# Optimization experiments

Hardware: AMD Instinct MI355X
Metric: run time of the kernel (lower is better)

Reference implementation:

```python
import jax, jax.numpy as jnp
import numpy as np


def setup_inputs() -> dict:
    key = jax.random.key(0)
    kK, kV, kQ = jax.random.split(key, 3)
    B, D, S = 4, 64, 4096
    K = jax.random.normal(kK, (B, D, S), dtype=jnp.float32)
    V = jax.random.normal(kV, (B, D, S), dtype=jnp.float32)
    Q = jax.random.normal(kQ, (B, D, S), dtype=jnp.float32)
    return {"K": K, "V": V, "Q": Q}


def reference(K, V, Q):
    # K,V: [B, D, Sk], Q: [B, D, Sq]
    d = Q.shape[1]
    # A[b,k,q] = sum_d K[b,d,k] * Q[b,d,q] / sqrt(d)
    A = jnp.einsum("bdk,bdq->bkq", K, Q) / jnp.sqrt(jnp.asarray(d, Q.dtype))
    A = jax.nn.softmax(A, axis=1)  # normalize over keys (dim 1), matching F.softmax(A, 1)
    # R[b,d,q] = sum_k V[b,d,k] * A[b,k,q]
    R = jnp.einsum("bdk,bkq->bdq", V, A)
    return jnp.concatenate((R, Q), axis=1)  # [B, 2D, Sq]
```

## Files before the change

kernel.cpp:

```cpp
#include <hip/hip_runtime.h>
#include <hip/hip_bf16.h>

#define S_LEN 4096
#define D_DIM 64
#define QB 64
#define KB 32
#define NT (S_LEN / KB)
#define TILE_E 4096
#define WT (NT / 8)

typedef __attribute__((ext_vector_type(8)))  short bf16x8;
typedef __attribute__((ext_vector_type(16))) float f32x16;
typedef unsigned int u32;

#define Z16 {0.f,0.f,0.f,0.f,0.f,0.f,0.f,0.f,0.f,0.f,0.f,0.f,0.f,0.f,0.f,0.f}

union bpack8 { __hip_bfloat16 h[8]; bf16x8 v; };
union ppack  { u32 w[4]; bf16x8 v; };

static __device__ __forceinline__ float fexp2(float x) {
    return __builtin_amdgcn_exp2f(x);
}
static __device__ __forceinline__ u32 cvtpk(float lo, float hi) {
    u32 r;
    asm("v_cvt_pk_bf16_f32 %0, %1, %2" : "=v"(r) : "v"(lo), "v"(hi));
    return r;
}
static __device__ __forceinline__ void plswap(u32 &a, u32 &b) {
    asm("v_permlane32_swap_b32 %0, %1" : "+v"(a), "+v"(b));
}

struct pfrag { ppack p0, p1; };
static __device__ __forceinline__ pfrag packP(const f32x16& s) {
    u32 A = cvtpk(s[0],  s[1]),  Bw = cvtpk(s[2],  s[3]);
    u32 C = cvtpk(s[4],  s[5]),  Dw = cvtpk(s[6],  s[7]);
    u32 E = cvtpk(s[8],  s[9]),  F  = cvtpk(s[10], s[11]);
    u32 G = cvtpk(s[12], s[13]), H  = cvtpk(s[14], s[15]);
    plswap(A, C); plswap(Bw, Dw); plswap(E, G); plswap(F, H);
    pfrag r;
    r.p0.w[0] = A; r.p0.w[1] = Bw; r.p0.w[2] = C; r.p0.w[3] = Dw;
    r.p1.w[0] = E; r.p1.w[1] = F;  r.p1.w[2] = G; r.p1.w[3] = H;
    return r;
}
static __device__ __forceinline__ float treesum(const f32x16& s) {
    float a0 = (s[0] + s[1])   + (s[2] + s[3]);
    float a1 = (s[4] + s[5])   + (s[6] + s[7]);
    float a2 = (s[8] + s[9])   + (s[10] + s[11]);
    float a3 = (s[12] + s[13]) + (s[14] + s[15]);
    return (a0 + a1) + (a2 + a3);
}

#define GLD16(gp, lp) __builtin_amdgcn_global_load_lds( \
    (const __attribute__((address_space(1))) u32*)(const void*)(gp), \
    (__attribute__((address_space(3))) u32*)(void*)(lp), 16, 0, 0)

#define QSCALE 0.18033688011112042f

__global__ __launch_bounds__(256)
void prep_kv(const float* __restrict__ K, const float* __restrict__ V,
             __hip_bfloat16* __restrict__ KVbf)
{
    const int b = blockIdx.y, x = blockIdx.x, z = blockIdx.z;
    const int t = threadIdx.x;

    if (z == 0) {
        const int key = t & 31, dg = t >> 5;
        const float* src = K + ((size_t)b * D_DIM + dg * 8) * S_LEN + x * KB + key;
        bpack8 u;
        #pragma unroll
        for (int e = 0; e < 8; ++e)
            u.h[e] = __float2bfloat16(src[(size_t)e * S_LEN]);
        *(bf16x8*)&KVbf[((size_t)b * NT + x) * TILE_E + t * 8] = u.v;
    } else {
        const int d = t >> 2, kg = t & 3;
        const float* p = V + ((size_t)b * D_DIM + d) * S_LEN + x * KB + kg * 8;
        float4 a = *(const float4*)p, c = *(const float4*)(p + 4);
        bpack8 u;
        u.h[0] = __float2bfloat16(a.x); u.h[1] = __float2bfloat16(a.y);
        u.h[2] = __float2bfloat16(a.z); u.h[3] = __float2bfloat16(a.w);
        u.h[4] = __float2bfloat16(c.x); u.h[5] = __float2bfloat16(c.y);
        u.h[6] = __float2bfloat16(c.z); u.h[7] = __float2bfloat16(c.w);
        *(bf16x8*)&KVbf[((size_t)b * NT + x) * TILE_E + 2048 + (kg * 64 + d) * 8] = u.v;
    }
}

__global__ __launch_bounds__(512, 2)
void attn_fwd(const __hip_bfloat16* __restrict__ KVbf,
              const float* __restrict__ Qg,
              float* __restrict__ out, int swz)
{
    int b, q0;
    if (swz) {
        const int blk = blockIdx.x;
        const int xcd = blk & 7;
        b  = xcd >> 1;
        q0 = (((xcd & 1) << 5) + (blk >> 3)) * QB;
    } else {
        b  = blockIdx.y;
        q0 = blockIdx.x * QB;
    }
    const int t  = threadIdx.x;
    const int lane = t & 63;
    const int w    = t >> 6;
    const int l5   = lane & 31;
    const int h    = lane >> 5;

    __shared__ __align__(16) char Ls[131072];
    char* myL = Ls + w * 16384;

    const __hip_bfloat16* kvb = KVbf + ((size_t)b * NT + w * WT) * TILE_E;
    const float* Qblk = Qg + (size_t)b * D_DIM * S_LEN + q0;

    {
        float* QF = (float*)Ls;
        #pragma unroll
        for (int i = 0; i < 8; ++i) {
            int d = i * 8 + w;
            QF[d * 65 + lane] = Qblk[(size_t)d * S_LEN + lane] * QSCALE;
        }
        __syncthreads();
    }
    bf16x8 qfA[4], qfB[4];
    {
        const float* QF = (const float*)Ls;
        #pragma unroll
        for (int j = 0; j < 4; ++j) {
            float a[8], bq[8];
            #pragma unroll
            for (int e = 0; e < 8; ++e) {
                int dabs = (2 * j + h) * 8 + e;
                a[e]  = QF[dabs * 65 + l5];
                bq[e] = QF[dabs * 65 + 32 + l5];
            }
            ppack pa, pb;
            #pragma unroll
            for (int k2 = 0; k2 < 4; ++k2) {
                pa.w[k2] = cvtpk(a[2 * k2],  a[2 * k2 + 1]);
                pb.w[k2] = cvtpk(bq[2 * k2], bq[2 * k2 + 1]);
            }
            qfA[j] = pa.v;
            qfB[j] = pb.v;
        }
        __syncthreads();
    }

    #pragma unroll
    for (int i = 0; i < 8; ++i)
        GLD16(kvb + i * 512 + lane * 8,          myL + i * 1024);
    #pragma unroll
    for (int i = 0; i < 8; ++i)
        GLD16(kvb + TILE_E + i * 512 + lane * 8, myL + 8192 + i * 1024);

    float lsumA = 0.f, lsumB = 0.f;
    f32x16 accA[2] = {Z16, Z16}, accB[2] = {Z16, Z16};

    for (int it = 0; it < WT; ++it) {
        if (it + 1 < WT) asm volatile("s_waitcnt vmcnt(8)" ::: "memory");
        else             asm volatile("s_waitcnt vmcnt(0)" ::: "memory");
        __builtin_amdgcn_sched_barrier(0);

        const char* Lk = myL + (it & 1) * 8192;
        const char* Lv = Lk + 4096;

        bf16x8 kf[4], vf[4];
        #pragma unroll
        for (int j = 0; j < 4; ++j)
            kf[j] = *(const bf16x8*)(Lk + ((2 * j + h) * 32 + l5) * 16);
        #pragma unroll
        for (int j = 0; j < 2; ++j)
            #pragma unroll
            for (int dt = 0; dt < 2; ++dt)
                vf[2 * j + dt] = *(const bf16x8*)(Lv + ((2 * j + h) * 64 + dt * 32 + l5) * 16);

        f32x16 sA = Z16, sB = Z16;
        __builtin_amdgcn_s_setprio(1);
        #pragma unroll
        for (int j = 0; j < 4; ++j) {
            sA = __builtin_amdgcn_mfma_f32_32x32x16_bf16(kf[j], qfA[j], sA, 0, 0, 0);
            sB = __builtin_amdgcn_mfma_f32_32x32x16_bf16(kf[j], qfB[j], sB, 0, 0, 0);
        }
        __builtin_amdgcn_s_setprio(0);

        if (it + 2 < WT) {
            asm volatile("s_waitcnt lgkmcnt(0)" ::: "memory");
            __builtin_amdgcn_sched_barrier(0);
            const __hip_bfloat16* nx = kvb + (size_t)(it + 2) * TILE_E;
            #pragma unroll
            for (int i = 0; i < 8; ++i)
                GLD16(nx + i * 512 + lane * 8, myL + (it & 1) * 8192 + i * 1024);
        }

        #pragma unroll
        for (int r = 0; r < 16; ++r) sA[r] = fexp2(sA[r]);
        #pragma unroll
        for (int r = 0; r < 16; ++r) sB[r] = fexp2(sB[r]);
        lsumA += treesum(sA);
        lsumB += treesum(sB);

        pfrag pA = packP(sA), pB = packP(sB);

        __builtin_amdgcn_s_setprio(1);
        #pragma unroll
        for (int j = 0; j < 2; ++j)
            #pragma unroll
            for (int dt = 0; dt < 2; ++dt) {
                const bf16x8 vv = vf[2 * j + dt];
                const ppack& pa = j ? pA.p1 : pA.p0;
                const ppack& pb = j ? pB.p1 : pB.p0;
                accA[dt] = __builtin_amdgcn_mfma_f32_32x32x16_bf16(vv, pa.v, accA[dt], 0, 0, 0);
                accB[dt] = __builtin_amdgcn_mfma_f32_32x32x16_bf16(vv, pb.v, accB[dt], 0, 0, 0);
            }
        __builtin_amdgcn_s_setprio(0);
    }

    lsumA += __shfl_xor(lsumA, 32);
    lsumB += __shfl_xor(lsumB, 32);

    float* LF = (float*)Ls;
    __syncthreads();
    if (h == 0) {
        LF[w * 64 + l5]      = lsumA;
        LF[w * 64 + 32 + l5] = lsumB;
    }
    __syncthreads();
    const int qp = t & 63;
    float den = 0.f;
    #pragma unroll
    for (int w2 = 0; w2 < 8; ++w2) den += LF[w2 * 64 + qp];
    const float inv = 1.f / den;
    __syncthreads();

    #pragma unroll
    for (int dt = 0; dt < 2; ++dt)
        #pragma unroll
        for (int r = 0; r < 16; ++r) {
            int d = dt * 32 + (r & 3) + 8 * (r >> 2) + 4 * h;
            LF[w * 2048 + d * 32 + l5]         = accA[dt][r];
            LF[16384 + w * 2048 + d * 32 + l5] = accB[dt][r];
        }
    __syncthreads();

    const int dgrp = t >> 6;
    const int slab = (qp < 32) ? 0 : 16384;
    const int qs   = qp & 31;
    float* op = out + (size_t)b * 2 * D_DIM * S_LEN + q0 + qp;
    #pragma unroll
    for (int dd = 0; dd < 8; ++dd) {
        int d = dgrp * 8 + dd;
        float sum = 0.f;
        #pragma unroll
        for (int w2 = 0; w2 < 8; ++w2)
            sum += LF[slab + w2 * 2048 + d * 32 + qs];
        op[(size_t)d * S_LEN] = sum * inv;
    }

    {
        float* oq = out + ((size_t)b * 2 * D_DIM + D_DIM) * S_LEN + q0;
        #pragma unroll
        for (int i = 0; i < 8; ++i) {
            int d = i * 8 + w;
            oq[(size_t)d * S_LEN + lane] = Qblk[(size_t)d * S_LEN + lane];
        }
    }
}

extern "C" void kernel_launch(void* const* d_in, const int* in_sizes, int n_in,
                              void* d_out, int out_size, void* d_ws, size_t ws_size,
                              hipStream_t stream) {
    const float* K = (const float*)d_in[0];
    const float* V = (const float*)d_in[1];
    const float* Q = (const float*)d_in[2];
    float* out = (float*)d_out;

    const int B = in_sizes[0] / (D_DIM * S_LEN);
    __hip_bfloat16* KVbf = (__hip_bfloat16*)d_ws;

    prep_kv<<<dim3(NT, B, 2), dim3(256), 0, stream>>>(K, V, KVbf);

    if (B == 4) {
        attn_fwd<<<dim3(256), dim3(512), 0, stream>>>(KVbf, Q, out, 1);
    } else {
        attn_fwd<<<dim3(S_LEN / QB, B), dim3(512), 0, stream>>>(KVbf, Q, out, 0);
    }
}
```

Before: 34.18 us.

## Software-pipeline QK MFMA one tile ahead of softmax and PV

Restructures the per-wave key loop so that the QK^T MFMAs for tile it+1 are issued before the exp/sum/pack and PV MFMAs of tile it, with a peeled prologue for the first tile. The global-to-LDS prefetch distance shifts to it+3 to match, and the loop is fully unrolled. The aim is to overlap the transcendental and packing VALU work with matrix-core work and hide LDS latency. In exchange it holds extra score and V-fragment registers live, which may raise VGPR pressure and code size.

Measured after the change: 33.12 us, median of 2. 3.1% less time.

```diff
diff --git a/kernel.cpp b/kernel.cpp
--- a/kernel.cpp
+++ b/kernel.cpp
@@ -144,6 +144,8 @@
         __syncthreads();
     }
 
+    const f32x16 ZV = Z16;
+
     #pragma unroll
     for (int i = 0; i < 8; ++i)
         GLD16(kvb + i * 512 + lane * 8,          myL + i * 1024);
@@ -151,66 +153,100 @@
     for (int i = 0; i < 8; ++i)
         GLD16(kvb + TILE_E + i * 512 + lane * 8, myL + 8192 + i * 1024);
 
+    asm volatile("s_waitcnt vmcnt(8)" ::: "memory");
+    __builtin_amdgcn_sched_barrier(0);
+
+    bf16x8 vfC[4], vfN[4], kfT[4];
+    f32x16 sAc = ZV, sBc = ZV, sAn, sBn;
     float lsumA = 0.f, lsumB = 0.f;
     f32x16 accA[2] = {Z16, Z16}, accB[2] = {Z16, Z16};
 
+    {
+        const char* Lk = myL;
+        const char* Lv = myL + 4096;
+        #pragma unroll
+        for (int j = 0; j < 4; ++j)
+            kfT[j] = *(const bf16x8*)(Lk + ((2 * j + h) * 32 + l5) * 16);
+        #pragma unroll
+        for (int j = 0; j < 2; ++j)
+            #pragma unroll
+            for (int dt = 0; dt < 2; ++dt)
+                vfC[2 * j + dt] = *(const bf16x8*)(Lv + ((2 * j + h) * 64 + dt * 32 + l5) * 16);
+        asm volatile("s_waitcnt lgkmcnt(0)" ::: "memory");
+        __builtin_amdgcn_sched_barrier(0);
+        __builtin_amdgcn_s_setprio(1);
+        #pragma unroll
+        for (int j = 0; j < 4; ++j) {
+            sAc = __builtin_amdgcn_mfma_f32_32x32x16_bf16(kfT[j], qfA[j], sAc, 0, 0, 0);
+            sBc = __builtin_amdgcn_mfma_f32_32x32x16_bf16(kfT[j], qfB[j], sBc, 0, 0, 0);
+        }
+        __builtin_amdgcn_s_setprio(0);
+        #pragma unroll
+        for (int i = 0; i < 8; ++i)
+            GLD16(kvb + 2 * (size_t)TILE_E + i * 512 + lane * 8, myL + i * 1024);
+    }
+
+    #pragma unroll
     for (int it = 0; it < WT; ++it) {
-        if (it + 1 < WT) asm volatile("s_waitcnt vmcnt(8)" ::: "memory");
-        else             asm volatile("s_waitcnt vmcnt(0)" ::: "memory");
-        __builtin_amdgcn_sched_barrier(0);
-
-        const char* Lk = myL + (it & 1) * 8192;
-        const char* Lv = Lk + 4096;
-
-        bf16x8 kf[4], vf[4];
-        #pragma unroll
-        for (int j = 0; j < 4; ++j)
-            kf[j] = *(const bf16x8*)(Lk + ((2 * j + h) * 32 + l5) * 16);
-        #pragma unroll
-        for (int j = 0; j < 2; ++j)
-            #pragma unroll
-            for (int dt = 0; dt < 2; ++dt)
-                vf[2 * j + dt] = *(const bf16x8*)(Lv + ((2 * j + h) * 64 + dt * 32 + l5) * 16);
-
-        f32x16 sA = Z16, sB = Z16;
-        __builtin_amdgcn_s_setprio(1);
-        #pragma unroll
-        for (int j = 0; j < 4; ++j) {
-            sA = __builtin_amdgcn_mfma_f32_32x32x16_bf16(kf[j], qfA[j], sA, 0, 0, 0);
-            sB = __builtin_amdgcn_mfma_f32_32x32x16_bf16(kf[j], qfB[j], sB, 0, 0, 0);
-        }
-        __builtin_amdgcn_s_setprio(0);
-
-        if (it + 2 < WT) {
+        if (it + 1 < WT) {
+            if (it + 2 < WT) { asm volatile("s_waitcnt vmcnt(8)" ::: "memory"); }
+            else             { asm volatile("s_waitcnt vmcnt(0)" ::: "memory"); }
+            __builtin_amdgcn_sched_barrier(0);
+            const char* Lk = myL + ((it + 1) & 1) * 8192;
+            const char* Lv = Lk + 4096;
+            #pragma unroll
+            for (int j = 0; j < 4; ++j)
+                kfT[j] = *(const bf16x8*)(Lk + ((2 * j + h) * 32 + l5) * 16);
+            #pragma unroll
+            for (int j = 0; j < 2; ++j)
+                #pragma unroll
+                for (int dt = 0; dt < 2; ++dt)
+                    vfN[2 * j + dt] = *(const bf16x8*)(Lv + ((2 * j + h) * 64 + dt * 32 + l5) * 16);
             asm volatile("s_waitcnt lgkmcnt(0)" ::: "memory");
             __builtin_amdgcn_sched_barrier(0);
-            const __hip_bfloat16* nx = kvb + (size_t)(it + 2) * TILE_E;
-            #pragma unroll
-            for (int i = 0; i < 8; ++i)
-                GLD16(nx + i * 512 + lane * 8, myL + (it & 1) * 8192 + i * 1024);
-        }
-
-        #pragma unroll
-        for (int r = 0; r < 16; ++r) sA[r] = fexp2(sA[r]);
-        #pragma unroll
-        for (int r = 0; r < 16; ++r) sB[r] = fexp2(sB[r]);
-        lsumA += treesum(sA);
-        lsumB += treesum(sB);
-
-        pfrag pA = packP(sA), pB = packP(sB);
+            sAn = ZV; sBn = ZV;
+            __builtin_amdgcn_s_setprio(1);
+            #pragma unroll
+            for (int j = 0; j < 4; ++j) {
+                sAn = __builtin_amdgcn_mfma_f32_32x32x16_bf16(kfT[j], qfA[j], sAn, 0, 0, 0);
+                sBn = __builtin_amdgcn_mfma_f32_32x32x16_bf16(kfT[j], qfB[j], sBn, 0, 0, 0);
+            }
+            __builtin_amdgcn_s_setprio(0);
+            if (it + 3 < WT) {
+                const __hip_bfloat16* nx = kvb + (size_t)(it + 3) * TILE_E;
+                #pragma unroll
+                for (int i = 0; i < 8; ++i)
+                    GLD16(nx + i * 512 + lane * 8, myL + ((it + 1) & 1) * 8192 + i * 1024);
+            }
+        }
+
+        #pragma unroll
+        for (int r = 0; r < 16; ++r) sAc[r] = fexp2(sAc[r]);
+        #pragma unroll
+        for (int r = 0; r < 16; ++r) sBc[r] = fexp2(sBc[r]);
+        lsumA += treesum(sAc);
+        lsumB += treesum(sBc);
+
+        pfrag pA = packP(sAc), pB = packP(sBc);
 
         __builtin_amdgcn_s_setprio(1);
         #pragma unroll
         for (int j = 0; j < 2; ++j)
             #pragma unroll
             for (int dt = 0; dt < 2; ++dt) {
-                const bf16x8 vv = vf[2 * j + dt];
+                const bf16x8 vv = vfC[2 * j + dt];
                 const ppack& pa = j ? pA.p1 : pA.p0;
                 const ppack& pb = j ? pB.p1 : pB.p0;
                 accA[dt] = __builtin_amdgcn_mfma_f32_32x32x16_bf16(vv, pa.v, accA[dt], 0, 0, 0);
                 accB[dt] = __builtin_amdgcn_mfma_f32_32x32x16_bf16(vv, pb.v, accB[dt], 0, 0, 0);
             }
         __builtin_amdgcn_s_setprio(0);
+
+        if (it + 1 < WT) {
+            sAc = sAn; sBc = sBn;
+            #pragma unroll
+            for (int j = 0; j < 4; ++j) vfC[j] = vfN[j];
+        }
     }
 
     lsumA += __shfl_xor(lsumA, 32);
```
